# Performance work log

Measured on AMD Instinct MI355X. Metric: run time of the kernel, lower is better.

Reference implementation:

```python
import jax, jax.numpy as jnp
import numpy as np

B, S, V, E, H, O = 256, 128, 50000, 256, 512, 32


def _cell(x, h, c, Wih, Whh, bih, bhh):
    # PyTorch LSTM gate order: i, f, g, o
    g = x @ Wih.T + h @ Whh.T + bih + bhh
    i, f, gg, o = jnp.split(g, 4, axis=-1)
    c = jax.nn.sigmoid(f) * c + jax.nn.sigmoid(i) * jnp.tanh(gg)
    h = jax.nn.sigmoid(o) * jnp.tanh(c)
    return h, c


def setup_inputs() -> dict:
    key = jax.random.key(0)
    ks = iter(jax.random.split(key, 32))
    n = lambda shape: jax.random.normal(next(ks), shape, dtype=jnp.float32) * 0.05
    return {
        'x': jax.random.randint(next(ks), (B, S), 0, V),
        'emb': n((V, E)),
        'enc_Wih0': n((4 * H, E)), 'enc_Whh0': n((4 * H, H)),
        'enc_bih0': n((4 * H,)), 'enc_bhh0': n((4 * H,)),
        'enc_Wih1': n((4 * H, H)), 'enc_Whh1': n((4 * H, H)),
        'enc_bih1': n((4 * H,)), 'enc_bhh1': n((4 * H,)),
        'dec_Wih0': n((4 * H, O)), 'dec_Whh0': n((4 * H, H)),
        'dec_bih0': n((4 * H,)), 'dec_bhh0': n((4 * H,)),
        'dec_Wih1': n((4 * H, H)), 'dec_Whh1': n((4 * H, H)),
        'dec_bih1': n((4 * H,)), 'dec_bhh1': n((4 * H,)),
        'fc_w': n((S, O, H)), 'fc_b': n((S, O)),
    }


def reference(x, emb, enc_Wih0, enc_Whh0, enc_bih0, enc_bhh0,
              enc_Wih1, enc_Whh1, enc_bih1, enc_bhh1,
              dec_Wih0, dec_Whh0, dec_bih0, dec_bhh0,
              dec_Wih1, dec_Whh1, dec_bih1, dec_bhh1,
              fc_w, fc_b):
    b = x.shape[0]
    xe = jnp.swapaxes(emb[x], 0, 1)  # [S, B, E]
    z = jnp.zeros((b, H), jnp.float32)

    # 2-layer LSTM encoder (eval mode: no dropout)
    def enc0(carry, xi):
        h, c = _cell(xi, carry[0], carry[1], enc_Wih0, enc_Whh0, enc_bih0, enc_bhh0)
        return (h, c), h
    (h0, c0), y0 = jax.lax.scan(enc0, (z, z), xe)

    def enc1(carry, xi):
        h, c = _cell(xi, carry[0], carry[1], enc_Wih1, enc_Whh1, enc_bih1, enc_bhh1)
        return (h, c), h
    (h1, c1), _ = jax.lax.scan(enc1, (z, z), y0)

    # greedy decoder: one-hot of previous argmax fed back each step
    in0 = jnp.zeros((b, O), jnp.float32).at[:, 0].set(1.0)

    def dec(carry, wb):
        h0, c0, h1, c1, xin = carry
        w, bb = wb  # per-step Linear: w [O, H], bb [O]
        h0, c0 = _cell(xin, h0, c0, dec_Wih0, dec_Whh0, dec_bih0, dec_bhh0)
        h1, c1 = _cell(h0, h1, c1, dec_Wih1, dec_Whh1, dec_bih1, dec_bhh1)
        probs = jax.nn.softmax(h1 @ w.T + bb, axis=-1)  # [B, O]
        nxt = jax.nn.one_hot(jnp.argmax(probs, axis=-1), O, dtype=probs.dtype)
        return (h0, c0, h1, c1, nxt), probs

    _, out = jax.lax.scan(dec, (h0, c0, h1, c1, in0), (fc_w, fc_b))
    return jnp.swapaxes(out, 0, 1)  # [B, S, O]
```

## Files before the change

### kernel.cpp

```cpp
#include <hip/hip_runtime.h>


#define BN 256
#define SN 128
#define EN 256
#define HN 512
#define ON 32
#define RG 32
#define NCG 32
#define NTHREADS 256
#define XSTR 264
#define HSTR 520
#define FSTR 520
#define GSTR 68
#define POLL_GUARD (1 << 20)
#define SLB 128

typedef _Float16 f16;
typedef _Float16 f16x8 __attribute__((ext_vector_type(8)));
typedef _Float16 f16x4 __attribute__((ext_vector_type(4)));
typedef _Float16 f16x2 __attribute__((ext_vector_type(2)));
typedef float f32x4 __attribute__((ext_vector_type(4)));
typedef unsigned u32x4 __attribute__((ext_vector_type(4)));

__device__ __forceinline__ f32x4 MFMA16(f16x8 a, f16x8 b, f32x4 c) {
  return __builtin_amdgcn_mfma_f32_16x16x32_f16(a, b, c, 0, 0, 0);
}

__device__ __forceinline__ float sigf(float x) { return 1.0f / (1.0f + __expf(-x)); }

template<int NKT>
__device__ __forceinline__ void loadW(const float* __restrict__ Wb, int K, int col, int quad,
                                      f16x8* dst) {
  #pragma unroll
  for (int kt = 0; kt < NKT; ++kt) {
    const float* p = Wb + (size_t)col * K + kt * 32 + quad * 8;
    f32x4 a = *(const f32x4*)p;
    f32x4 b = *(const f32x4*)(p + 4);
    f16x8 h;
    h[0] = (f16)a[0]; h[1] = (f16)a[1]; h[2] = (f16)a[2]; h[3] = (f16)a[3];
    h[4] = (f16)b[0]; h[5] = (f16)b[1]; h[6] = (f16)b[2]; h[7] = (f16)b[3];
    dst[kt] = h;
  }
}

__device__ __forceinline__ void issue8(u32x4* v, const char* __restrict__ src, int tid) {
  const char* base = src + tid * 16;
  #pragma unroll
  for (int j = 0; j < 8; ++j)
    asm volatile("global_load_dwordx4 %0, %1, off sc1" : "=v"(v[j]) : "v"(base + j * 4096));
}
__device__ __forceinline__ void write8(f16* dst, const u32x4* v, int tid) {
  #pragma unroll
  for (int j = 0; j < 8; ++j) {
    int u = j * 256 + tid, rr = u >> 6, cc = u & 63;
    *(u32x4*)&dst[rr * HSTR + cc * 8] = v[j];
  }
}

template<int NKT>
__device__ __forceinline__ void matmulAcc(f32x4* acc, const f16* stage, int stride,
                                          const f16x8* Wr, int l16, int quad) {
  #pragma unroll
  for (int mt = 0; mt < 2; ++mt) {
    #pragma unroll
    for (int kt = 0; kt < NKT; ++kt) {
      f16x8 a = *(const f16x8*)&stage[(mt * 16 + l16) * stride + kt * 32 + quad * 8];
      acc[mt] = MFMA16(a, Wr[kt], acc[mt]);
    }
  }
}

__device__ __forceinline__ void arrive_flag(int* slots, int g, int cg, int tid, int rnd) {
  asm volatile("s_waitcnt vmcnt(0)" ::: "memory");
  __syncthreads();
  if (tid == 0)
    __hip_atomic_store(&slots[g * SLB + ((rnd & 1) ? 64 : 96) + cg], rnd,
                       __ATOMIC_RELAXED, __HIP_MEMORY_SCOPE_AGENT);
}

__device__ __forceinline__ void wait_flag(int* slots, int g, int tid, int rnd, int* esc) {
  if (!*esc) {
    const int* p = &slots[g * SLB + ((rnd & 1) ? 64 : 96) + (tid & 31)];
    int gd = 0;
    for (;;) {
      int v = __hip_atomic_load(p, __ATOMIC_RELAXED, __HIP_MEMORY_SCOPE_AGENT);
      if (__all(v == rnd)) break;
      if (++gd > POLL_GUARD) { *esc = 1; break; }
      __builtin_amdgcn_s_sleep(1);
    }
  }
  asm volatile("" ::: "memory");
}

__device__ __forceinline__ void gatherXE(f16* xes, const int* __restrict__ xTok,
                                         const float* __restrict__ emb, int g, int k, int tid) {
  int r = tid & 31, sub = tid >> 5;
  int tok = xTok[(g * RG + r) * SN + k];
  const float* er = emb + (size_t)tok * EN + sub * 32;
  f16* dst = &xes[r * XSTR + sub * 32];
  #pragma unroll
  for (int jj = 0; jj < 32; jj += 8) {
    f32x4 a = *(const f32x4*)(er + jj);
    f32x4 b = *(const f32x4*)(er + jj + 4);
    f16x8 hv;
    hv[0] = (f16)a[0]; hv[1] = (f16)a[1]; hv[2] = (f16)a[2]; hv[3] = (f16)a[3];
    hv[4] = (f16)b[0]; hv[5] = (f16)b[1]; hv[6] = (f16)b[2]; hv[7] = (f16)b[3];
    *(f16x8*)(dst + jj) = hv;
  }
}

__device__ __forceinline__ void stageFCW(f16* fcwb, const float* __restrict__ fcw,
                                         int st, int tid) {
  const float* base = fcw + (size_t)st * ON * HN;
  #pragma unroll
  for (int j = 0; j < 16; ++j) {
    int fo = (tid + j * 256) * 4;
    int col = fo >> 9, k = fo & 511;
    f32x4 a = *(const f32x4*)(base + fo);
    f16x4 hv;
    hv[0] = (f16)a[0]; hv[1] = (f16)a[1]; hv[2] = (f16)a[2]; hv[3] = (f16)a[3];
    *(f16x4*)&fcwb[col * FSTR + k] = hv;
  }
}

__device__ __forceinline__ void pointwise_store(const float* gb, int row, int d0, float* cv,
                                                unsigned* __restrict__ hout, int g, int cg,
                                                int sub) {
  const float* gr = gb + row * GSTR + d0;
  union { unsigned u; f16x2 h; } hv;
  #pragma unroll
  for (int j = 0; j < 2; ++j) {
    float vi = gr[j], vf = gr[16 + j], vg = gr[32 + j], vo = gr[48 + j];
    cv[j] = sigf(vf) * cv[j] + sigf(vi) * tanhf(vg);
    hv.h[j] = (f16)(sigf(vo) * tanhf(cv[j]));
  }
  __hip_atomic_store(&hout[(g * RG + row) * 256 + cg * 8 + sub], hv.u,
                     __ATOMIC_RELAXED, __HIP_MEMORY_SCOPE_AGENT);
}

__launch_bounds__(NTHREADS, 1)
__global__ void lstm_all(const int* __restrict__ xTok, const float* __restrict__ emb,
    const float* __restrict__ eWih0, const float* __restrict__ eWhh0,
    const float* __restrict__ ebih0, const float* __restrict__ ebhh0,
    const float* __restrict__ eWih1, const float* __restrict__ eWhh1,
    const float* __restrict__ ebih1, const float* __restrict__ ebhh1,
    const float* __restrict__ dWih0, const float* __restrict__ dWhh0,
    const float* __restrict__ dbih0, const float* __restrict__ dbhh0,
    const float* __restrict__ dWih1, const float* __restrict__ dWhh1,
    const float* __restrict__ dbih1, const float* __restrict__ dbhh1,
    const float* __restrict__ fcw, const float* __restrict__ fcb,
    float* __restrict__ dout, char* __restrict__ h0buf, char* __restrict__ h1buf,
    int* __restrict__ slots)
{
  __shared__ __align__(16) char upool[RG * XSTR * 2];
  __shared__ __align__(16) f16 h0s[RG * HSTR];
  __shared__ __align__(16) f16 h1s[RG * HSTR];
  __shared__ __align__(16) f16 fcwb[ON * FSTR];
  __shared__ float gbuf0[RG * GSTR];
  __shared__ float gbuf1[RG * GSTR];
  __shared__ int amaxlds[RG];
  __shared__ int esc;

  f16*   xes  = (f16*)upool;
  float* lbuf = (float*)upool;
  float* w0d  = (float*)(upool + 4352);

  const int tid  = threadIdx.x;
  const int g    = blockIdx.x & 7;
  const int cg   = blockIdx.x >> 3;
  const int w    = tid >> 6;
  const int lane = tid & 63;
  const int quad = lane >> 4;
  const int l16  = lane & 15;
  const int colg = w * HN + cg * 16 + l16;
  const int urow = tid >> 3;
  const int ud0  = (tid & 7) * 2;
  int rnd = 0;
  if (tid == 0) esc = 0;

  f16x8 Wi0r[8], Wh0r[16], Wi1r[16], Wh1r[16];
  loadW<8>(eWih0, EN, colg, quad, Wi0r);
  loadW<16>(eWhh0, HN, colg, quad, Wh0r);
  loadW<16>(eWih1, HN, colg, quad, Wi1r);
  loadW<16>(eWhh1, HN, colg, quad, Wh1r);
  float bias0 = ebih0[colg] + ebhh0[colg];
  float bias1 = ebih1[colg] + ebhh1[colg];

  gatherXE(xes, xTok, emb, g, 0, tid);
  float c0[2] = {0.f, 0.f}, c1[2] = {0.f, 0.f};
  {
    unsigned idx = (unsigned)(BN * 256 + (g * RG + urow) * 256 + cg * 8 + (tid & 7));
    __hip_atomic_store((unsigned*)h0buf + idx, 0u, __ATOMIC_RELAXED, __HIP_MEMORY_SCOPE_AGENT);
    __hip_atomic_store((unsigned*)h1buf + idx, 0u, __ATOMIC_RELAXED, __HIP_MEMORY_SCOPE_AGENT);
  }
  asm volatile("s_waitcnt vmcnt(0)" ::: "memory");
  __syncthreads();
  if (tid == 0) {
    __hip_atomic_store(&slots[g * SLB + 64 + cg], 0, __ATOMIC_RELAXED, __HIP_MEMORY_SCOPE_AGENT);
    __hip_atomic_store(&slots[g * SLB + 96 + cg], 0, __ATOMIC_RELAXED, __HIP_MEMORY_SCOPE_AGENT);
    asm volatile("s_waitcnt vmcnt(0)" ::: "memory");
    __hip_atomic_store(&slots[g * SLB + cg], 1, __ATOMIC_RELAXED, __HIP_MEMORY_SCOPE_AGENT);
  }
  if (!esc) {
    int idx = tid & 31;
    int gd = 0;
    for (;;) {
      int v = __hip_atomic_load(&slots[g * SLB + idx], __ATOMIC_RELAXED,
                                __HIP_MEMORY_SCOPE_AGENT);
      if (__all(v >= 1)) break;
      if (++gd > POLL_GUARD) { esc = 1; break; }
      __builtin_amdgcn_s_sleep(1);
    }
  }
  __syncthreads();

  for (int k = 0; k <= SN; ++k) {
    u32x4 v0[8], v1[8];
    issue8(v0, h0buf + (size_t)((k - 1) & 1) * BN * HN * 2 + (size_t)(g * RG) * HN * 2, tid);
    if (k >= 1)
      issue8(v1, h1buf + (size_t)(k & 1) * BN * HN * 2 + (size_t)(g * RG) * HN * 2, tid);

    f32x4 acc0[2], acc1[2];
    if (k < SN) {
      f32x4 b0; b0[0] = bias0; b0[1] = bias0; b0[2] = bias0; b0[3] = bias0;
      acc0[0] = b0; acc0[1] = b0;
      matmulAcc<8>(acc0, xes, XSTR, Wi0r, l16, quad);
    }
    if (k >= 1) asm volatile("s_waitcnt vmcnt(8)" ::: "memory");
    else        asm volatile("s_waitcnt vmcnt(0)" ::: "memory");
    write8(h0s, v0, tid);
    __syncthreads();
    if (k < SN) matmulAcc<16>(acc0, h0s, HSTR, Wh0r, l16, quad);
    if (k >= 1) {
      f32x4 b1; b1[0] = bias1; b1[1] = bias1; b1[2] = bias1; b1[3] = bias1;
      acc1[0] = b1; acc1[1] = b1;
      matmulAcc<16>(acc1, h0s, HSTR, Wi1r, l16, quad);
      asm volatile("s_waitcnt vmcnt(0)" ::: "memory");
      write8(h1s, v1, tid);
      __syncthreads();
      matmulAcc<16>(acc1, h1s, HSTR, Wh1r, l16, quad);
    }

    #pragma unroll
    for (int mt = 0; mt < 2; ++mt) {
      #pragma unroll
      for (int i = 0; i < 4; ++i) {
        int rr = (mt * 16 + quad * 4 + i) * GSTR + w * 16 + l16;
        if (k < SN) gbuf0[rr] = acc0[mt][i];
        if (k >= 1) gbuf1[rr] = acc1[mt][i];
      }
    }
    __syncthreads();
    if (k < SN)
      pointwise_store(gbuf0, urow, ud0, c0,
                      (unsigned*)(h0buf + (size_t)(k & 1) * BN * HN * 2), g, cg, tid & 7);
    if (k >= 1)
      pointwise_store(gbuf1, urow, ud0, c1,
                      (unsigned*)(h1buf + (size_t)((k - 1) & 1) * BN * HN * 2), g, cg, tid & 7);

    ++rnd;
    arrive_flag(slots, g, cg, tid, rnd);
    if (k < SN - 1) gatherXE(xes, xTok, emb, g, k + 1, tid);
    __syncthreads();
    wait_flag(slots, g, tid, rnd, &esc);
  }

  loadW<16>(dWhh0, HN, colg, quad, Wh0r);
  loadW<16>(dWih1, HN, colg, quad, Wi1r);
  loadW<16>(dWhh1, HN, colg, quad, Wh1r);
  bias0 = dbih0[colg] + dbhh0[colg];
  bias1 = dbih1[colg] + dbhh1[colg];
  {
    int cl = tid >> 2, i0 = (tid & 3) * 8;
    int gcol = (cl >> 4) * HN + cg * 16 + (cl & 15);
    const float* p = dWih0 + (size_t)gcol * ON + i0;
    #pragma unroll
    for (int j = 0; j < 8; ++j) w0d[cl * 32 + i0 + j] = p[j];
  }
  if (tid < RG) amaxlds[tid] = 0;

  for (int t = 0; t <= SN; ++t) {
    u32x4 v0[8];
    issue8(v0, h1buf + (size_t)((t - 1) & 1) * BN * HN * 2 + (size_t)(g * RG) * HN * 2, tid);
    float fb = 0.f;
    if (t >= 1) fb = fcb[(t - 1) * ON + ((w >> 1) * 16 + l16)];

    f32x4 acc0[2];
    if (t < SN) {
      acc0[0] = f32x4{0.f, 0.f, 0.f, 0.f}; acc0[1] = acc0[0];
      matmulAcc<16>(acc0, h0s, HSTR, Wh0r, l16, quad);
    }
    asm volatile("s_waitcnt vmcnt(0)" ::: "memory");
    write8(h1s, v0, tid);
    __syncthreads();

    if (t >= 1) {
      int fmt = w & 1, fnt = w >> 1;
      int colo = fnt * 16 + l16;
      f32x4 afc = {0.f, 0.f, 0.f, 0.f};
      #pragma unroll
      for (int kt = 0; kt < 16; ++kt) {
        f16x8 bf = *(const f16x8*)&fcwb[colo * FSTR + kt * 32 + quad * 8];
        f16x8 av = *(const f16x8*)&h1s[(fmt * 16 + l16) * HSTR + kt * 32 + quad * 8];
        afc = MFMA16(av, bf, afc);
      }
      #pragma unroll
      for (int i = 0; i < 4; ++i)
        lbuf[(fmt * 16 + quad * 4 + i) * 33 + colo] = afc[i] + fb;
      __syncthreads();
      {
        int st = t - 1;
        int row = tid >> 3, s = tid & 7, cbase = s * 4;
        float vv[4];
        #pragma unroll
        for (int j = 0; j < 4; ++j) vv[j] = lbuf[row * 33 + cbase + j];
        float mx = vv[0]; int bi = cbase;
        #pragma unroll
        for (int j = 1; j < 4; ++j)
          if (vv[j] > mx) { mx = vv[j]; bi = cbase + j; }
        #pragma unroll
        for (int m = 1; m < 8; m <<= 1) {
          float om = __shfl_xor(mx, m);
          int   ob = __shfl_xor(bi, m);
          if (om > mx || (om == mx && ob < bi)) { mx = om; bi = ob; }
        }
        float e[4], ss = 0.f;
        #pragma unroll
        for (int j = 0; j < 4; ++j) { e[j] = __expf(vv[j] - mx); ss += e[j]; }
        #pragma unroll
        for (int m = 1; m < 8; m <<= 1) ss += __shfl_xor(ss, m);
        if (s == 0) amaxlds[row] = bi;
        if (cg == 0) {
          float inv = 1.0f / ss;
          float* op = dout + ((size_t)(g * RG + row) * SN + st) * ON + cbase;
          #pragma unroll
          for (int j = 0; j < 4; ++j) op[j] = e[j] * inv;
        }
      }
      __syncthreads();
    }

    if (t < SN) {
      #pragma unroll
      for (int mt = 0; mt < 2; ++mt) {
        #pragma unroll
        for (int i = 0; i < 4; ++i) {
          int row = mt * 16 + quad * 4 + i;
          acc0[mt][i] += bias0 + w0d[(w * 16 + l16) * 32 + amaxlds[row]];
        }
      }
      #pragma unroll
      for (int mt = 0; mt < 2; ++mt) {
        #pragma unroll
        for (int i = 0; i < 4; ++i)
          gbuf0[(mt * 16 + quad * 4 + i) * GSTR + w * 16 + l16] = acc0[mt][i];
      }
      __syncthreads();
      pointwise_store(gbuf0, urow, ud0, c0,
                      (unsigned*)(h0buf + (size_t)(t & 1) * BN * HN * 2), g, cg, tid & 7);
    }
    ++rnd;
    arrive_flag(slots, g, cg, tid, rnd);
    wait_flag(slots, g, tid, rnd, &esc);

    if (t < SN) {
      u32x4 v2[8];
      issue8(v2, h0buf + (size_t)(t & 1) * BN * HN * 2 + (size_t)(g * RG) * HN * 2, tid);
      f32x4 acc1[2];
      f32x4 b1; b1[0] = bias1; b1[1] = bias1; b1[2] = bias1; b1[3] = bias1;
      acc1[0] = b1; acc1[1] = b1;
      matmulAcc<16>(acc1, h1s, HSTR, Wh1r, l16, quad);
      asm volatile("s_waitcnt vmcnt(0)" ::: "memory");
      write8(h0s, v2, tid);
      __syncthreads();
      matmulAcc<16>(acc1, h0s, HSTR, Wi1r, l16, quad);
      #pragma unroll
      for (int mt = 0; mt < 2; ++mt) {
        #pragma unroll
        for (int i = 0; i < 4; ++i)
          gbuf0[(mt * 16 + quad * 4 + i) * GSTR + w * 16 + l16] = acc1[mt][i];
      }
      __syncthreads();
      pointwise_store(gbuf0, urow, ud0, c1,
                      (unsigned*)(h1buf + (size_t)(t & 1) * BN * HN * 2), g, cg, tid & 7);
      ++rnd;
      arrive_flag(slots, g, cg, tid, rnd);
      stageFCW(fcwb, fcw, t, tid);
      __syncthreads();
      wait_flag(slots, g, tid, rnd, &esc);
    }
  }
}

extern "C" void kernel_launch(void* const* d_in, const int* in_sizes, int n_in,
                              void* d_out, int out_size, void* d_ws, size_t ws_size,
                              hipStream_t stream) {
  (void)in_sizes; (void)n_in; (void)out_size; (void)ws_size;
  const int*   xTok  = (const int*)d_in[0];
  const float* emb   = (const float*)d_in[1];
  const float* eWih0 = (const float*)d_in[2];
  const float* eWhh0 = (const float*)d_in[3];
  const float* ebih0 = (const float*)d_in[4];
  const float* ebhh0 = (const float*)d_in[5];
  const float* eWih1 = (const float*)d_in[6];
  const float* eWhh1 = (const float*)d_in[7];
  const float* ebih1 = (const float*)d_in[8];
  const float* ebhh1 = (const float*)d_in[9];
  const float* dWih0 = (const float*)d_in[10];
  const float* dWhh0 = (const float*)d_in[11];
  const float* dbih0 = (const float*)d_in[12];
  const float* dbhh0 = (const float*)d_in[13];
  const float* dWih1 = (const float*)d_in[14];
  const float* dWhh1 = (const float*)d_in[15];
  const float* dbih1 = (const float*)d_in[16];
  const float* dbhh1 = (const float*)d_in[17];
  const float* fcw   = (const float*)d_in[18];
  const float* fcb   = (const float*)d_in[19];

  char* h0buf = (char*)d_ws;
  char* h1buf = (char*)d_ws + (size_t)2 * BN * HN * 2;
  int*  slots = (int*)((char*)d_ws + (size_t)4 * BN * HN * 2);

  hipLaunchKernelGGL(lstm_all, dim3(256), dim3(NTHREADS), 0, stream,
                     xTok, emb, eWih0, eWhh0, ebih0, ebhh0, eWih1, eWhh1, ebih1, ebhh1,
                     dWih0, dWhh0, dbih0, dbhh0, dWih1, dWhh1, dbih1, dbhh1,
                     fcw, fcb, (float*)d_out, h0buf, h1buf, slots);
}
```

Measured before the change: 2.922 ms.

## Split row groups into two half-groups pipelined with counter-based barriers

```diff
diff --git a/kernel.cpp b/kernel.cpp
--- a/kernel.cpp
+++ b/kernel.cpp
@@ -7,6 +7,7 @@
 #define HN 512
 #define ON 32
 #define RG 32
+#define RS 16
 #define NCG 32
 #define NTHREADS 256
 #define XSTR 264
@@ -44,48 +45,46 @@
   }
 }
 
-__device__ __forceinline__ void issue8(u32x4* v, const char* __restrict__ src, int tid) {
+__device__ __forceinline__ void issue4(u32x4* v, const char* __restrict__ src, int tid) {
   const char* base = src + tid * 16;
   #pragma unroll
-  for (int j = 0; j < 8; ++j)
+  for (int j = 0; j < 4; ++j)
     asm volatile("global_load_dwordx4 %0, %1, off sc1" : "=v"(v[j]) : "v"(base + j * 4096));
 }
-__device__ __forceinline__ void write8(f16* dst, const u32x4* v, int tid) {
-  #pragma unroll
-  for (int j = 0; j < 8; ++j) {
+__device__ __forceinline__ void write4(f16* dst, const u32x4* v, int tid) {
+  #pragma unroll
+  for (int j = 0; j < 4; ++j) {
     int u = j * 256 + tid, rr = u >> 6, cc = u & 63;
     *(u32x4*)&dst[rr * HSTR + cc * 8] = v[j];
   }
 }
 
 template<int NKT>
-__device__ __forceinline__ void matmulAcc(f32x4* acc, const f16* stage, int stride,
-                                          const f16x8* Wr, int l16, int quad) {
-  #pragma unroll
-  for (int mt = 0; mt < 2; ++mt) {
-    #pragma unroll
-    for (int kt = 0; kt < NKT; ++kt) {
-      f16x8 a = *(const f16x8*)&stage[(mt * 16 + l16) * stride + kt * 32 + quad * 8];
-      acc[mt] = MFMA16(a, Wr[kt], acc[mt]);
-    }
-  }
-}
-
-__device__ __forceinline__ void arrive_flag(int* slots, int g, int cg, int tid, int rnd) {
-  asm volatile("s_waitcnt vmcnt(0)" ::: "memory");
+__device__ __forceinline__ void matmul1(f32x4& acc, const f16* stage, int stride,
+                                        const f16x8* Wr, int l16, int quad) {
+  #pragma unroll
+  for (int kt = 0; kt < NKT; ++kt) {
+    f16x8 a = *(const f16x8*)&stage[l16 * stride + kt * 32 + quad * 8];
+    acc = MFMA16(a, Wr[kt], acc);
+  }
+}
+
+__device__ __forceinline__ void arriveS(int* slots, int g, int soff, int tid) {
   __syncthreads();
-  if (tid == 0)
-    __hip_atomic_store(&slots[g * SLB + ((rnd & 1) ? 64 : 96) + cg], rnd,
-                       __ATOMIC_RELAXED, __HIP_MEMORY_SCOPE_AGENT);
-}
-
-__device__ __forceinline__ void wait_flag(int* slots, int g, int tid, int rnd, int* esc) {
+  if (tid == 0) {
+    asm volatile("s_waitcnt vmcnt(0)" ::: "memory");
+    int one = 1;
+    int* p = &slots[g * SLB + soff];
+    asm volatile("global_atomic_add %0, %1, off" :: "v"(p), "v"(one) : "memory");
+  }
+}
+__device__ __forceinline__ void waitS(int* slots, int g, int soff, int target, int* esc) {
   if (!*esc) {
-    const int* p = &slots[g * SLB + ((rnd & 1) ? 64 : 96) + (tid & 31)];
+    const int* p = &slots[g * SLB + soff];
     int gd = 0;
     for (;;) {
       int v = __hip_atomic_load(p, __ATOMIC_RELAXED, __HIP_MEMORY_SCOPE_AGENT);
-      if (__all(v == rnd)) break;
+      if (v >= target) break;
       if (++gd > POLL_GUARD) { *esc = 1; break; }
       __builtin_amdgcn_s_sleep(1);
     }
@@ -93,14 +92,15 @@
   asm volatile("" ::: "memory");
 }
 
-__device__ __forceinline__ void gatherXE(f16* xes, const int* __restrict__ xTok,
-                                         const float* __restrict__ emb, int g, int k, int tid) {
-  int r = tid & 31, sub = tid >> 5;
-  int tok = xTok[(g * RG + r) * SN + k];
-  const float* er = emb + (size_t)tok * EN + sub * 32;
-  f16* dst = &xes[r * XSTR + sub * 32];
-  #pragma unroll
-  for (int jj = 0; jj < 32; jj += 8) {
+__device__ __forceinline__ void gatherXE(f16* xs, const int* __restrict__ xTok,
+                                         const float* __restrict__ emb, int g, int s, int k,
+                                         int tid) {
+  int r = tid & 15, sub = tid >> 4;
+  int tok = xTok[(g * RG + s * RS + r) * SN + k];
+  const float* er = emb + (size_t)tok * EN + sub * 16;
+  f16* dst = &xs[r * XSTR + sub * 16];
+  #pragma unroll
+  for (int jj = 0; jj < 16; jj += 8) {
     f32x4 a = *(const f32x4*)(er + jj);
     f32x4 b = *(const f32x4*)(er + jj + 4);
     f16x8 hv;
@@ -124,10 +124,11 @@
   }
 }
 
-__device__ __forceinline__ void pointwise_store(const float* gb, int row, int d0, float* cv,
-                                                unsigned* __restrict__ hout, int g, int cg,
-                                                int sub) {
-  const float* gr = gb + row * GSTR + d0;
+__device__ __forceinline__ void pointwise16(const float* gb, float* cv,
+                                            unsigned* __restrict__ hout, int rowbase,
+                                            int cg, int tid) {
+  int row = tid >> 3, sub = tid & 7;
+  const float* gr = gb + row * GSTR + sub * 2;
   union { unsigned u; f16x2 h; } hv;
   #pragma unroll
   for (int j = 0; j < 2; ++j) {
@@ -135,7 +136,7 @@
     cv[j] = sigf(vf) * cv[j] + sigf(vi) * tanhf(vg);
     hv.h[j] = (f16)(sigf(vo) * tanhf(cv[j]));
   }
-  __hip_atomic_store(&hout[(g * RG + row) * 256 + cg * 8 + sub], hv.u,
+  __hip_atomic_store(&hout[(rowbase + row) * 256 + cg * 8 + sub], hv.u,
                      __ATOMIC_RELAXED, __HIP_MEMORY_SCOPE_AGENT);
 }
 
@@ -153,18 +154,18 @@
     float* __restrict__ dout, char* __restrict__ h0buf, char* __restrict__ h1buf,
     int* __restrict__ slots)
 {
-  __shared__ __align__(16) char upool[RG * XSTR * 2];
-  __shared__ __align__(16) f16 h0s[RG * HSTR];
-  __shared__ __align__(16) f16 h1s[RG * HSTR];
+  __shared__ __align__(16) f16 h0s[2 * RS * HSTR];
+  __shared__ __align__(16) f16 h1s[2 * RS * HSTR];
+  __shared__ __align__(16) f16 xes[2 * RS * XSTR];
   __shared__ __align__(16) f16 fcwb[ON * FSTR];
-  __shared__ float gbuf0[RG * GSTR];
-  __shared__ float gbuf1[RG * GSTR];
+  __shared__ float gbuf0[RS * GSTR];
+  __shared__ float gbuf1[RS * GSTR];
+  __shared__ __align__(16) char upool[2176 + 8192];
   __shared__ int amaxlds[RG];
   __shared__ int esc;
 
-  f16*   xes  = (f16*)upool;
   float* lbuf = (float*)upool;
-  float* w0d  = (float*)(upool + 4352);
+  float* w0d  = (float*)(upool + 2176);
 
   const int tid  = threadIdx.x;
   const int g    = blockIdx.x & 7;
@@ -174,9 +175,7 @@
   const int quad = lane >> 4;
   const int l16  = lane & 15;
   const int colg = w * HN + cg * 16 + l16;
-  const int urow = tid >> 3;
-  const int ud0  = (tid & 7) * 2;
-  int rnd = 0;
+  int ct[2] = {0, 0};
   if (tid == 0) esc = 0;
 
   f16x8 Wi0r[8], Wh0r[16], Wi1r[16], Wh1r[16];
@@ -187,9 +186,12 @@
   float bias0 = ebih0[colg] + ebhh0[colg];
   float bias1 = ebih1[colg] + ebhh1[colg];
 
-  gatherXE(xes, xTok, emb, g, 0, tid);
-  float c0[2] = {0.f, 0.f}, c1[2] = {0.f, 0.f};
+  gatherXE(&xes[0],             xTok, emb, g, 0, 0, tid);
+  gatherXE(&xes[RS * XSTR],     xTok, emb, g, 1, 0, tid);
+  float c0s[2][2] = {{0.f, 0.f}, {0.f, 0.f}};
+  float c1s[2][2] = {{0.f, 0.f}, {0.f, 0.f}};
   {
+    int urow = tid >> 3;
     unsigned idx = (unsigned)(BN * 256 + (g * RG + urow) * 256 + cg * 8 + (tid & 7));
     __hip_atomic_store((unsigned*)h0buf + idx, 0u, __ATOMIC_RELAXED, __HIP_MEMORY_SCOPE_AGENT);
     __hip_atomic_store((unsigned*)h1buf + idx, 0u, __ATOMIC_RELAXED, __HIP_MEMORY_SCOPE_AGENT);
@@ -197,8 +199,8 @@
   asm volatile("s_waitcnt vmcnt(0)" ::: "memory");
   __syncthreads();
   if (tid == 0) {
-    __hip_atomic_store(&slots[g * SLB + 64 + cg], 0, __ATOMIC_RELAXED, __HIP_MEMORY_SCOPE_AGENT);
-    __hip_atomic_store(&slots[g * SLB + 96 + cg], 0, __ATOMIC_RELAXED, __HIP_MEMORY_SCOPE_AGENT);
+    __hip_atomic_store(&slots[g * SLB + 64], 0, __ATOMIC_RELAXED, __HIP_MEMORY_SCOPE_AGENT);
+    __hip_atomic_store(&slots[g * SLB + 96], 0, __ATOMIC_RELAXED, __HIP_MEMORY_SCOPE_AGENT);
     asm volatile("s_waitcnt vmcnt(0)" ::: "memory");
     __hip_atomic_store(&slots[g * SLB + cg], 1, __ATOMIC_RELAXED, __HIP_MEMORY_SCOPE_AGENT);
   }
@@ -216,54 +218,60 @@
   __syncthreads();
 
   for (int k = 0; k <= SN; ++k) {
-    u32x4 v0[8], v1[8];
-    issue8(v0, h0buf + (size_t)((k - 1) & 1) * BN * HN * 2 + (size_t)(g * RG) * HN * 2, tid);
-    if (k >= 1)
-      issue8(v1, h1buf + (size_t)(k & 1) * BN * HN * 2 + (size_t)(g * RG) * HN * 2, tid);
-
-    f32x4 acc0[2], acc1[2];
-    if (k < SN) {
-      f32x4 b0; b0[0] = bias0; b0[1] = bias0; b0[2] = bias0; b0[3] = bias0;
-      acc0[0] = b0; acc0[1] = b0;
-      matmulAcc<8>(acc0, xes, XSTR, Wi0r, l16, quad);
-    }
-    if (k >= 1) asm volatile("s_waitcnt vmcnt(8)" ::: "memory");
-    else        asm volatile("s_waitcnt vmcnt(0)" ::: "memory");
-    write8(h0s, v0, tid);
-    __syncthreads();
-    if (k < SN) matmulAcc<16>(acc0, h0s, HSTR, Wh0r, l16, quad);
-    if (k >= 1) {
-      f32x4 b1; b1[0] = bias1; b1[1] = bias1; b1[2] = bias1; b1[3] = bias1;
-      acc1[0] = b1; acc1[1] = b1;
-      matmulAcc<16>(acc1, h0s, HSTR, Wi1r, l16, quad);
-      asm volatile("s_waitcnt vmcnt(0)" ::: "memory");
-      write8(h1s, v1, tid);
+    #pragma unroll
+    for (int s = 0; s < 2; ++s) {
+      const int soff = 64 + s * 32;
+      f16* h0ss = &h0s[s * RS * HSTR];
+      f16* h1ss = &h1s[s * RS * HSTR];
+      f16* xss  = &xes[s * RS * XSTR];
+      const size_t rbyte = (size_t)(g * RG + s * RS) * HN * 2;
+
+      waitS(slots, g, soff, ct[s], &esc);
+
+      u32x4 v0[4], v1[4];
+      issue4(v0, h0buf + (size_t)((k - 1) & 1) * BN * HN * 2 + rbyte, tid);
+      if (k >= 1)
+        issue4(v1, h1buf + (size_t)(k & 1) * BN * HN * 2 + rbyte, tid);
+
+      f32x4 a0, a1;
+      if (k < SN) {
+        a0[0] = bias0; a0[1] = bias0; a0[2] = bias0; a0[3] = bias0;
+        matmul1<8>(a0, xss, XSTR, Wi0r, l16, quad);
+      }
+      if (k >= 1) asm volatile("s_waitcnt vmcnt(4)" ::: "memory");
+      else        asm volatile("s_waitcnt vmcnt(0)" ::: "memory");
+      write4(h0ss, v0, tid);
       __syncthreads();
-      matmulAcc<16>(acc1, h1s, HSTR, Wh1r, l16, quad);
-    }
-
-    #pragma unroll
-    for (int mt = 0; mt < 2; ++mt) {
+      if (k < SN) matmul1<16>(a0, h0ss, HSTR, Wh0r, l16, quad);
+      if (k >= 1) {
+        a1[0] = bias1; a1[1] = bias1; a1[2] = bias1; a1[3] = bias1;
+        matmul1<16>(a1, h0ss, HSTR, Wi1r, l16, quad);
+        asm volatile("s_waitcnt vmcnt(0)" ::: "memory");
+        write4(h1ss, v1, tid);
+        __syncthreads();
+        matmul1<16>(a1, h1ss, HSTR, Wh1r, l16, quad);
+      }
+
       #pragma unroll
       for (int i = 0; i < 4; ++i) {
-        int rr = (mt * 16 + quad * 4 + i) * GSTR + w * 16 + l16;
-        if (k < SN) gbuf0[rr] = acc0[mt][i];
-        if (k >= 1) gbuf1[rr] = acc1[mt][i];
-      }
+        int rr = (quad * 4 + i) * GSTR + w * 16 + l16;
+        if (k < SN) gbuf0[rr] = a0[i];
+        if (k >= 1) gbuf1[rr] = a1[i];
+      }
+      __syncthreads();
+      if (tid < 128) {
+        if (k < SN)
+          pointwise16(gbuf0, c0s[s], (unsigned*)(h0buf + (size_t)(k & 1) * BN * HN * 2),
+                      g * RG + s * RS, cg, tid);
+        if (k >= 1)
+          pointwise16(gbuf1, c1s[s], (unsigned*)(h1buf + (size_t)((k - 1) & 1) * BN * HN * 2),
+                      g * RG + s * RS, cg, tid);
+      }
+      arriveS(slots, g, soff, tid);
+      ct[s] += NCG;
+      if (k < SN - 1) gatherXE(xss, xTok, emb, g, s, k + 1, tid);
+      __syncthreads();
     }
-    __syncthreads();
-    if (k < SN)
-      pointwise_store(gbuf0, urow, ud0, c0,
-                      (unsigned*)(h0buf + (size_t)(k & 1) * BN * HN * 2), g, cg, tid & 7);
-    if (k >= 1)
-      pointwise_store(gbuf1, urow, ud0, c1,
-                      (unsigned*)(h1buf + (size_t)((k - 1) & 1) * BN * HN * 2), g, cg, tid & 7);
-
-    ++rnd;
-    arrive_flag(slots, g, cg, tid, rnd);
-    if (k < SN - 1) gatherXE(xes, xTok, emb, g, k + 1, tid);
-    __syncthreads();
-    wait_flag(slots, g, tid, rnd, &esc);
   }
 
   loadW<16>(dWhh0, HN, colg, quad, Wh0r);
@@ -279,116 +287,124 @@
     for (int j = 0; j < 8; ++j) w0d[cl * 32 + i0 + j] = p[j];
   }
   if (tid < RG) amaxlds[tid] = 0;
+  __syncthreads();
 
   for (int t = 0; t <= SN; ++t) {
-    u32x4 v0[8];
-    issue8(v0, h1buf + (size_t)((t - 1) & 1) * BN * HN * 2 + (size_t)(g * RG) * HN * 2, tid);
-    float fb = 0.f;
-    if (t >= 1) fb = fcb[(t - 1) * ON + ((w >> 1) * 16 + l16)];
-
-    f32x4 acc0[2];
-    if (t < SN) {
-      acc0[0] = f32x4{0.f, 0.f, 0.f, 0.f}; acc0[1] = acc0[0];
-      matmulAcc<16>(acc0, h0s, HSTR, Wh0r, l16, quad);
-    }
-    asm volatile("s_waitcnt vmcnt(0)" ::: "memory");
-    write8(h1s, v0, tid);
-    __syncthreads();
-
-    if (t >= 1) {
-      int fmt = w & 1, fnt = w >> 1;
-      int colo = fnt * 16 + l16;
-      f32x4 afc = {0.f, 0.f, 0.f, 0.f};
-      #pragma unroll
-      for (int kt = 0; kt < 16; ++kt) {
-        f16x8 bf = *(const f16x8*)&fcwb[colo * FSTR + kt * 32 + quad * 8];
-        f16x8 av = *(const f16x8*)&h1s[(fmt * 16 + l16) * HSTR + kt * 32 + quad * 8];
-        afc = MFMA16(av, bf, afc);
-      }
-      #pragma unroll
-      for (int i = 0; i < 4; ++i)
-        lbuf[(fmt * 16 + quad * 4 + i) * 33 + colo] = afc[i] + fb;
+    #pragma unroll
+    for (int s = 0; s < 2; ++s) {
+      const int soff = 64 + s * 32;
+      f16* h0ss = &h0s[s * RS * HSTR];
+      f16* h1ss = &h1s[s * RS * HSTR];
+      const size_t rbyte = (size_t)(g * RG + s * RS) * HN * 2;
+
+      waitS(slots, g, soff, ct[s], &esc);
+
+      u32x4 v0[4];
+      issue4(v0, h1buf + (size_t)((t - 1) & 1) * BN * HN * 2 + rbyte, tid);
+      f32x4 a0;
+      if (t < SN) {
+        a0[0] = 0.f; a0[1] = 0.f; a0[2] = 0.f; a0[3] = 0.f;
+        matmul1<16>(a0, h0ss, HSTR, Wh0r, l16, quad);
+      }
+      float fb = 0.f;
+      if (t >= 1 && w < 2) fb = fcb[(t - 1) * ON + w * 16 + l16];
+      asm volatile("s_waitcnt vmcnt(0)" ::: "memory");
+      write4(h1ss, v0, tid);
       __syncthreads();
-      {
-        int st = t - 1;
-        int row = tid >> 3, s = tid & 7, cbase = s * 4;
-        float vv[4];
+
+      if (t >= 1) {
+        if (w < 2) {
+          f32x4 afc = {0.f, 0.f, 0.f, 0.f};
+          #pragma unroll
+          for (int kt = 0; kt < 16; ++kt) {
+            f16x8 bf = *(const f16x8*)&fcwb[(w * 16 + l16) * FSTR + kt * 32 + quad * 8];
+            f16x8 av = *(const f16x8*)&h1ss[l16 * HSTR + kt * 32 + quad * 8];
+            afc = MFMA16(av, bf, afc);
+          }
+          #pragma unroll
+          for (int i = 0; i < 4; ++i)
+            lbuf[(quad * 4 + i) * 33 + w * 16 + l16] = afc[i] + fb;
+        }
+        __syncthreads();
+        if (tid < 128) {
+          int st = t - 1;
+          int row = tid >> 3, s8 = tid & 7, cbase = s8 * 4;
+          float vv[4];
+          #pragma unroll
+          for (int j = 0; j < 4; ++j) vv[j] = lbuf[row * 33 + cbase + j];
+          float mx = vv[0]; int bi = cbase;
+          #pragma unroll
+          for (int j = 1; j < 4; ++j)
+            if (vv[j] > mx) { mx = vv[j]; bi = cbase + j; }
+          #pragma unroll
+          for (int m = 1; m < 8; m <<= 1) {
+            float om = __shfl_xor(mx, m);
+            int   ob = __shfl_xor(bi, m);
+            if (om > mx || (om == mx && ob < bi)) { mx = om; bi = ob; }
+          }
+          float e[4], ss = 0.f;
+          #pragma unroll
+          for (int j = 0; j < 4; ++j) { e[j] = __expf(vv[j] - mx); ss += e[j]; }
+          #pragma unroll
+          for (int m = 1; m < 8; m <<= 1) ss += __shfl_xor(ss, m);
+          if (s8 == 0) amaxlds[s * RS + row] = bi;
+          if (cg == 0) {
+            float inv = 1.0f / ss;
+            float* op = dout + ((size_t)(g * RG + s * RS + row) * SN + st) * ON + cbase;
+            #pragma unroll
+            for (int j = 0; j < 4; ++j) op[j] = e[j] * inv;
+          }
+        }
+        __syncthreads();
+      }
+
+      if (t < SN) {
         #pragma unroll
-        for (int j = 0; j < 4; ++j) vv[j] = lbuf[row * 33 + cbase + j];
-        float mx = vv[0]; int bi = cbase;
+        for (int i = 0; i < 4; ++i)
+          a0[i] += bias0 + w0d[(w * 16 + l16) * 32 + amaxlds[s * RS + quad * 4 + i]];
         #pragma unroll
-        for (int j = 1; j < 4; ++j)
-          if (vv[j] > mx) { mx = vv[j]; bi = cbase + j; }
-        #pragma unroll
-        for (int m = 1; m < 8; m <<= 1) {
-          float om = __shfl_xor(mx, m);
-          int   ob = __shfl_xor(bi, m);
-          if (om > mx || (om == mx && ob < bi)) { mx = om; bi = ob; }
-        }
-        float e[4], ss = 0.f;
-        #pragma unroll
-        for (int j = 0; j < 4; ++j) { e[j] = __expf(vv[j] - mx); ss += e[j]; }
-        #pragma unroll
-        for (int m = 1; m < 8; m <<= 1) ss += __shfl_xor(ss, m);
-        if (s == 0) amaxlds[row] = bi;
-        if (cg == 0) {
-          float inv = 1.0f / ss;
-          float* op = dout + ((size_t)(g * RG + row) * SN + st) * ON + cbase;
-          #pragma unroll
-          for (int j = 0; j < 4; ++j) op[j] = e[j] * inv;
-        }
-      }
-      __syncthreads();
+        for (int i = 0; i < 4; ++i)
+          gbuf0[(quad * 4 + i) * GSTR + w * 16 + l16] = a0[i];
+        __syncthreads();
+        if (tid < 128)
+          pointwise16(gbuf0, c0s[s], (unsigned*)(h0buf + (size_t)(t & 1) * BN * HN * 2),
+                      g * RG + s * RS, cg, tid);
+      }
+      arriveS(slots, g, soff, tid);
+      ct[s] += NCG;
     }
 
     if (t < SN) {
       #pragma unroll
-      for (int mt = 0; mt < 2; ++mt) {
-        #pragma unroll
-        for (int i = 0; i < 4; ++i) {
-          int row = mt * 16 + quad * 4 + i;
-          acc0[mt][i] += bias0 + w0d[(w * 16 + l16) * 32 + amaxlds[row]];
-        }
-      }
-      #pragma unroll
-      for (int mt = 0; mt < 2; ++mt) {
+      for (int s = 0; s < 2; ++s) {
+        const int soff = 64 + s * 32;
+        f16* h0ss = &h0s[s * RS * HSTR];
+        f16* h1ss = &h1s[s * RS * HSTR];
+        const size_t rbyte = (size_t)(g * RG + s * RS) * HN * 2;
+
+        waitS(slots, g, soff, ct[s], &esc);
+
+        u32x4 v2[4];
+        issue4(v2, h0buf + (size_t)(t & 1) * BN * HN * 2 + rbyte, tid);
+        f32x4 a1;
+        a1[0] = bias1; a1[1] = bias1; a1[2] = bias1; a1[3] = bias1;
+        matmul1<16>(a1, h1ss, HSTR, Wh1r, l16, quad);
+        asm volatile("s_waitcnt vmcnt(0)" ::: "memory");
+        write4(h0ss, v2, tid);
+        __syncthreads();
+        matmul1<16>(a1, h0ss, HSTR, Wi1r, l16, quad);
         #pragma unroll
         for (int i = 0; i < 4; ++i)
-          gbuf0[(mt * 16 + quad * 4 + i) * GSTR + w * 16 + l16] = acc0[mt][i];
-      }
-      __syncthreads();
-      pointwise_store(gbuf0, urow, ud0, c0,
-                      (unsigned*)(h0buf + (size_t)(t & 1) * BN * HN * 2), g, cg, tid & 7);
-    }
-    ++rnd;
-    arrive_flag(slots, g, cg, tid, rnd);
-    wait_flag(slots, g, tid, rnd, &esc);
-
-    if (t < SN) {
-      u32x4 v2[8];
-      issue8(v2, h0buf + (size_t)(t & 1) * BN * HN * 2 + (size_t)(g * RG) * HN * 2, tid);
-      f32x4 acc1[2];
-      f32x4 b1; b1[0] = bias1; b1[1] = bias1; b1[2] = bias1; b1[3] = bias1;
-      acc1[0] = b1; acc1[1] = b1;
-      matmulAcc<16>(acc1, h1s, HSTR, Wh1r, l16, quad);
-      asm volatile("s_waitcnt vmcnt(0)" ::: "memory");
-      write8(h0s, v2, tid);
-      __syncthreads();
-      matmulAcc<16>(acc1, h0s, HSTR, Wi1r, l16, quad);
-      #pragma unroll
-      for (int mt = 0; mt < 2; ++mt) {
-        #pragma unroll
-        for (int i = 0; i < 4; ++i)
-          gbuf0[(mt * 16 + quad * 4 + i) * GSTR + w * 16 + l16] = acc1[mt][i];
-      }
-      __syncthreads();
-      pointwise_store(gbuf0, urow, ud0, c1,
-                      (unsigned*)(h1buf + (size_t)(t & 1) * BN * HN * 2), g, cg, tid & 7);
-      ++rnd;
-      arrive_flag(slots, g, cg, tid, rnd);
-      stageFCW(fcwb, fcw, t, tid);
-      __syncthreads();
-      wait_flag(slots, g, tid, rnd, &esc);
+          gbuf0[(quad * 4 + i) * GSTR + w * 16 + l16] = a1[i];
+        __syncthreads();
+        if (tid < 128)
+          pointwise16(gbuf0, c1s[s], (unsigned*)(h1buf + (size_t)(t & 1) * BN * HN * 2),
+                      g * RG + s * RS, cg, tid);
+        arriveS(slots, g, soff, tid);
+        ct[s] += NCG;
+        if (s == 0) stageFCW(fcwb, fcw, t, tid);
+        __syncthreads();
+      }
     }
   }
 }
```

Result: slower. 3.241 ms (+10.9%).
